# Kernel tuning notes

Measured on AMD Instinct MI355X. Metric: run time of the kernel, lower is better.

Reference implementation:

```python
import jax, jax.numpy as jnp
import numpy as np

B, S, HID, H = 4, 2048, 768, 12
D = HID // H  # 64
SCALE = 1.0 / (D ** 0.5)


def setup_inputs() -> dict:
    key = jax.random.key(0)
    ks = jax.random.split(key, 12)
    std = 0.02
    inp = {
        'Q': jax.random.normal(ks[0], (B, S, HID), jnp.float32),
        'K': jax.random.normal(ks[1], (B, S, HID), jnp.float32),
        'V': jax.random.normal(ks[2], (B, S, HID), jnp.float32),
        'attn_mask': jax.random.randint(ks[3], (B, S, S), 0, 2) == 1,
        'Wq': jax.random.normal(ks[4], (HID, HID), jnp.float32) * std,
        'bq': jnp.zeros((HID,), jnp.float32),
        'Wk': jax.random.normal(ks[5], (HID, HID), jnp.float32) * std,
        'bk': jnp.zeros((HID,), jnp.float32),
        'Wv': jax.random.normal(ks[6], (HID, HID), jnp.float32) * std,
        'bv': jnp.zeros((HID,), jnp.float32),
        'Wo': jax.random.normal(ks[7], (HID, HID), jnp.float32) * std,
        'bo': jnp.zeros((HID,), jnp.float32),
    }
    return inp


def reference(Q, K, V, attn_mask, Wq, bq, Wk, bk, Wv, bv, Wo, bo):
    b, s, _ = Q.shape
    # projections -> [b, h, s, d]
    def split_heads(x):
        return x.reshape(b, s, H, D).transpose(0, 2, 1, 3)
    q = split_heads(Q @ Wq + bq)
    k = split_heads(K @ Wk + bk)
    v = split_heads(V @ Wv + bv)
    # eager attention: materialize full [b,h,s,s] scores
    scores = jnp.einsum('bhqd,bhkd->bhqk', q, k) * SCALE
    scores = jnp.where(attn_mask[:, None, :, :], jnp.float32(-1e9), scores)
    attn_prob = jax.nn.softmax(scores, axis=-1)
    # dropout is identity in eval mode
    context = jnp.einsum('bhqk,bhkd->bhqd', attn_prob, v)
    context = context.transpose(0, 2, 1, 3).reshape(b, s, H * D)
    output = context @ Wo + bo
    return (output, attn_prob)
```

## Files before the change

kernel.cpp:

```cpp
#include <hip/hip_runtime.h>
#include <hip/hip_bf16.h>
#include <stdint.h>

#define BB 4
#define SS 2048
#define HIDD 768
#define HH 12
#define DD 64
#define SCALE_F 0.125f
#define NQKV ((size_t)BB * SS * HIDD)
#define NW ((size_t)HIDD * HIDD)
#define NMW ((size_t)BB * SS * (SS / 64))

using bf16 = __hip_bfloat16;
typedef __attribute__((ext_vector_type(8))) short short8v;
typedef __attribute__((ext_vector_type(4))) float f32x4;
typedef __attribute__((ext_vector_type(4))) float fvec4;
typedef __attribute__((ext_vector_type(4))) unsigned int uvec4;

__device__ __forceinline__ float ldf(const float* p, size_t i) { return p[i]; }
__device__ __forceinline__ float ldf(const bf16* p, size_t i) { return __bfloat162float(p[i]); }

__device__ __forceinline__ uint32_t bfb(float f) {
    bf16 h = __float2bfloat16(f);
    uint16_t u;
    __builtin_memcpy(&u, &h, 2);
    return (uint32_t)u;
}
__device__ __forceinline__ float b2f(uint32_t u) {
    uint32_t w = u << 16;
    float f;
    __builtin_memcpy(&f, &w, 4);
    return f;
}
__device__ __forceinline__ uint4 load8p(const float* p) {
    float4 a = *(const float4*)p;
    float4 b = *(const float4*)(p + 4);
    uint4 r;
    r.x = bfb(a.x) | (bfb(a.y) << 16);
    r.y = bfb(a.z) | (bfb(a.w) << 16);
    r.z = bfb(b.x) | (bfb(b.y) << 16);
    r.w = bfb(b.z) | (bfb(b.w) << 16);
    return r;
}

__device__ __forceinline__ short8v ldfrag(const char* base, int row, int bofs) {
    return *(const short8v*)(base + row * 128 + (bofs ^ ((row & 7) << 4)));
}

typedef __attribute__((address_space(1))) void as1_void;
typedef __attribute__((address_space(3))) void as3_void;
__device__ __forceinline__ void gload16(const void* g, void* l) {
    __builtin_amdgcn_global_load_lds((as1_void*)g, (as3_void*)l, 16, 0, 0);
}

__global__ void detect_kernel(const uint32_t* __restrict__ qraw,
                              const uint32_t* __restrict__ mraw,
                              int* __restrict__ flags) {
    __shared__ int ci, cn;
    int tid = threadIdx.x;
    if (tid == 0) { ci = 0; cn = 0; }
    __syncthreads();
    int li = 0;
    for (int l = 0; l < 8; l++) {
        uint32_t w = qraw[tid + l * 256];
        #pragma unroll
        for (int h = 0; h < 2; h++) {
            uint32_t bits = (h ? (w >> 16) : (w & 0xffffu)) << 16;
            float f = __uint_as_float(bits);
            float a = fabsf(f);
            if (a != 0.0f && (a > 1e3f || a < 1e-4f)) li++;
        }
    }
    int ln = 0;
    for (int l = 0; l < 4; l++) {
        if (mraw[tid + l * 256] > 1u) ln++;
    }
    atomicAdd(&ci, li);
    atomicAdd(&cn, ln);
    __syncthreads();
    if (tid == 0) {
        flags[0] = (ci > 1024) ? 0 : 1;
        flags[1] = (cn > 64) ? 1 : 0;
    }
}

__global__ __launch_bounds__(256) void bitpack_mask(const int* __restrict__ flags,
                                                    const void* __restrict__ maskp,
                                                    uint64_t* __restrict__ mbits) {
    int gw = (int)((blockIdx.x * 256 + threadIdx.x) >> 6);
    int lane = threadIdx.x & 63;
    int byteM = flags[1];
    const int* mi = (const int*)maskp;
    const uint8_t* mb = (const uint8_t*)maskp;
    for (int it = 0; it < 64; it++) {
        size_t wi = (size_t)gw * 64 + it;
        size_t e = wi * 64 + lane;
        int m = byteM ? (int)mb[e] : mi[e];
        unsigned long long b = __ballot(m != 0);
        if (lane == 0) mbits[wi] = (uint64_t)b;
    }
}

__global__ __launch_bounds__(256) void convert_in(const int* __restrict__ flags,
                                                  const void* __restrict__ Q,
                                                  const void* __restrict__ K,
                                                  const void* __restrict__ V,
                                                  bf16* __restrict__ xb) {
    int isbf = flags[0];
    int z = blockIdx.y;
    const void* src = (z == 0) ? Q : (z == 1) ? K : V;
    size_t base = ((size_t)blockIdx.x * 256 + threadIdx.x) * 8;
    bf16* dst = xb + (size_t)z * NQKV + base;
    if (isbf) {
        *(uint4*)dst = *(const uint4*)((const bf16*)src + base);
    } else {
        *(uint4*)dst = load8p((const float*)src + base);
    }
}

__global__ void convert_bias(const int* __restrict__ flags,
                             const void* __restrict__ b0, const void* __restrict__ b1,
                             const void* __restrict__ b2, const void* __restrict__ b3,
                             float* __restrict__ bf) {
    int isbf = flags[0];
    for (int i = threadIdx.x; i < 4 * HIDD; i += 256) {
        int z = i / HIDD, j = i - z * HIDD;
        const void* b = (z == 0) ? b0 : (z == 1) ? b1 : (z == 2) ? b2 : b3;
        bf[i] = isbf ? b2f((uint32_t) * ((const uint16_t*)b + j)) : ((const float*)b)[j];
    }
}

__global__ __launch_bounds__(256) void transpose_w2(const int* __restrict__ flags,
                                                    const void* __restrict__ W0,
                                                    const void* __restrict__ W1,
                                                    const void* __restrict__ W2,
                                                    const void* __restrict__ W3,
                                                    bf16* __restrict__ WT) {
    int isbf = flags[0];
    __shared__ uint16_t tb[64][65];
    int tid = threadIdx.x;
    int z = blockIdx.z;
    const void* W = (z == 0) ? W0 : (z == 1) ? W1 : (z == 2) ? W2 : W3;
    int k0 = blockIdx.y * 64, n0 = blockIdx.x * 64;
    #pragma unroll
    for (int l = 0; l < 16; l++) {
        int idx = tid + l * 256;
        int r = idx >> 6, c = idx & 63;
        size_t off = (size_t)(k0 + r) * HIDD + n0 + c;
        tb[c][r] = isbf ? *((const uint16_t*)W + off) : (uint16_t)bfb(((const float*)W)[off]);
    }
    __syncthreads();
    bf16* dst = WT + (size_t)z * NW;
    #pragma unroll
    for (int l = 0; l < 16; l++) {
        int idx = tid + l * 256;
        int r = idx >> 6, c = idx & 63;
        *(uint16_t*)&dst[(size_t)(n0 + r) * HIDD + k0 + c] = tb[r][c];
    }
}

template <int HSPLIT>
__global__ __launch_bounds__(256) void gemm3(const int* __restrict__ flags,
                                             const bf16* __restrict__ X,
                                             const bf16* __restrict__ WT,
                                             const float* __restrict__ biasf,
                                             bf16* __restrict__ Yh,
                                             float* __restrict__ Yf,
                                             bf16* __restrict__ Yb) {
    __shared__ char xs[128 * 128];
    __shared__ char ws[64 * 128];
    int tid = threadIdx.x;
    int lane = tid & 63, w = tid >> 6;
    int g = lane >> 4, t = lane & 15;
    int row0 = blockIdx.y * 128, n0 = blockIdx.x * 64;
    const f32x4 fz = {0.f, 0.f, 0.f, 0.f};
    f32x4 acc[2][4];
    #pragma unroll
    for (int rb = 0; rb < 2; rb++)
        #pragma unroll
        for (int c = 0; c < 4; c++) acc[rb][c] = fz;
    int r8 = tid >> 3, c8 = tid & 7;
    const char* Xb0 = (const char*)(X + (size_t)row0 * HIDD);
    const char* Wb0 = (const char*)(WT + (size_t)n0 * HIDD);
    for (int kt = 0; kt < HIDD; kt += 64) {
        #pragma unroll
        for (int i = 0; i < 4; i++) {
            int r = r8 + i * 32;
            gload16(Xb0 + (size_t)r * (HIDD * 2) + kt * 2 + ((c8 * 16) ^ ((r & 7) << 4)),
                    xs + w * 1024 + i * 4096);
        }
        #pragma unroll
        for (int i = 0; i < 2; i++) {
            int r = r8 + i * 32;
            gload16(Wb0 + (size_t)r * (HIDD * 2) + kt * 2 + ((c8 * 16) ^ ((r & 7) << 4)),
                    ws + w * 1024 + i * 4096);
        }
        __syncthreads();
        #pragma unroll
        for (int ks = 0; ks < 2; ks++) {
            short8v a0 = ldfrag(xs, w * 32 + t, g * 16 + ks * 64);
            short8v a1 = ldfrag(xs, w * 32 + 16 + t, g * 16 + ks * 64);
            #pragma unroll
            for (int c = 0; c < 4; c++) {
                short8v b = ldfrag(ws, c * 16 + t, g * 16 + ks * 64);
                acc[0][c] = __builtin_amdgcn_mfma_f32_16x16x32_bf16(a0, b, acc[0][c], 0, 0, 0);
                acc[1][c] = __builtin_amdgcn_mfma_f32_16x16x32_bf16(a1, b, acc[1][c], 0, 0, 0);
            }
        }
        __syncthreads();
    }
    int isbf = flags[0];
    #pragma unroll
    for (int c = 0; c < 4; c++) {
        int col = n0 + c * 16 + t;
        float bv = biasf[col];
        #pragma unroll
        for (int rb = 0; rb < 2; rb++) {
            #pragma unroll
            for (int r = 0; r < 4; r++) {
                int row = row0 + w * 32 + rb * 16 + g * 4 + r;
                float v = acc[rb][c][r] + bv;
                if (HSPLIT) {
                    int b_ = row >> 11, s = row & 2047, h2 = col >> 6, d = col & 63;
                    Yh[(((size_t)b_ * HH + h2) * SS + s) * DD + d] = __float2bfloat16(v);
                } else {
                    if (isbf) Yb[(size_t)row * HIDD + col] = __float2bfloat16(v);
                    else      Yf[(size_t)row * HIDD + col] = v;
                }
            }
        }
    }
}

__global__ __launch_bounds__(256) void transpose_v(const bf16* __restrict__ vh,
                                                   bf16* __restrict__ vt) {
    __shared__ uint16_t tb[64][65];
    int tid = threadIdx.x;
    int s0 = blockIdx.x * 64, bh = blockIdx.y;
    const bf16* src = vh + ((size_t)bh * SS + s0) * DD;
    #pragma unroll
    for (int i = 0; i < 2; i++) {
        int u = tid + (i << 8);
        int r = u >> 3, sg = u & 7;
        uint4 v = *(const uint4*)(src + (size_t)r * DD + sg * 8);
        uint32_t wv[4] = {v.x, v.y, v.z, v.w};
        #pragma unroll
        for (int j = 0; j < 4; j++) {
            tb[r][sg * 8 + 2 * j]     = (uint16_t)(wv[j] & 0xffffu);
            tb[r][sg * 8 + 2 * j + 1] = (uint16_t)(wv[j] >> 16);
        }
    }
    __syncthreads();
    bf16* dst = vt + (size_t)bh * DD * SS + s0;
    #pragma unroll
    for (int i = 0; i < 2; i++) {
        int u = tid + (i << 8);
        int d = u >> 3, sg = u & 7;
        uint32_t w0 = (uint32_t)tb[sg * 8 + 0][d] | ((uint32_t)tb[sg * 8 + 1][d] << 16);
        uint32_t w1 = (uint32_t)tb[sg * 8 + 2][d] | ((uint32_t)tb[sg * 8 + 3][d] << 16);
        uint32_t w2 = (uint32_t)tb[sg * 8 + 4][d] | ((uint32_t)tb[sg * 8 + 5][d] << 16);
        uint32_t w3 = (uint32_t)tb[sg * 8 + 6][d] | ((uint32_t)tb[sg * 8 + 7][d] << 16);
        uint4 o; o.x = w0; o.y = w1; o.z = w2; o.w = w3;
        *(uint4*)(dst + (size_t)d * SS + sg * 8) = o;
    }
}

__global__ __launch_bounds__(256) void fused_attn3(const int* __restrict__ flags,
                                                   const bf16* __restrict__ qh,
                                                   const bf16* __restrict__ kh,
                                                   const bf16* __restrict__ vt,
                                                   const uint64_t* __restrict__ mbits,
                                                   float* __restrict__ Pf,
                                                   bf16* __restrict__ Ph,
                                                   bf16* __restrict__ ctx) {
    const int isf32 = (flags[0] == 0);
    __shared__ char pl[16 * 4096];
    __shared__ float red[4][16];
    __shared__ float invl[16];
    int tid = threadIdx.x;
    int lane = tid & 63, w = tid >> 6;
    int g = lane >> 4, t = lane & 15;
    int q0 = blockIdx.x * 16, bh = blockIdx.y;
    int b_ = bh / HH, h = bh - b_ * HH;
    const f32x4 fz = {0.f, 0.f, 0.f, 0.f};
    int bitIdx = w * 16 + t;

    const bf16* qbase = qh + ((size_t)bh * SS + q0 + t) * DD;
    short8v aq0 = *(const short8v*)(qbase + g * 8);
    short8v aq1 = *(const short8v*)(qbase + 32 + g * 8);

    const bf16* kcol = kh + ((size_t)bh * SS + bitIdx) * DD + g * 8;
    const bf16* vrow = vt + ((size_t)bh * DD + bitIdx) * SS + g * 8;
    const uint64_t* mrowp[4];
    #pragma unroll
    for (int r = 0; r < 4; r++)
        mrowp[r] = mbits + ((size_t)b_ * SS + q0 + g * 4 + r) * (SS / 64);

    short8v cK0 = *(const short8v*)(kcol);
    short8v cK1 = *(const short8v*)(kcol + 32);
    short8v cV0 = *(const short8v*)(vrow);
    short8v cV1 = *(const short8v*)(vrow + 32);
    uint64_t cM[4];
    #pragma unroll
    for (int r = 0; r < 4; r++) cM[r] = mrowp[r][0];

    float sum4[4] = {0.f, 0.f, 0.f, 0.f};
    f32x4 o = fz;

    for (int kt = 0; kt < SS; kt += 64) {
        int ktn = (kt + 64) & (SS - 1);
        const bf16* kn = kcol + (size_t)ktn * DD;
        const bf16* vn = vrow + ktn;
        short8v nK0 = *(const short8v*)(kn);
        short8v nK1 = *(const short8v*)(kn + 32);
        short8v nV0 = *(const short8v*)(vn);
        short8v nV1 = *(const short8v*)(vn + 32);
        int wn = ((kt >> 6) + 1) & 31;
        uint64_t nM[4];
        #pragma unroll
        for (int r = 0; r < 4; r++) nM[r] = mrowp[r][wn];

        f32x4 s = fz;
        s = __builtin_amdgcn_mfma_f32_16x16x32_bf16(aq0, cK0, s, 0, 0, 0);
        s = __builtin_amdgcn_mfma_f32_16x16x32_bf16(aq1, cK1, s, 0, 0, 0);

        #pragma unroll
        for (int r = 0; r < 4; r++) {
            int msk = (int)((cM[r] >> bitIdx) & 1ull);
            float sv = msk ? -1e30f : s[r] * SCALE_F;
            float p = __expf(fminf(sv, 30.0f));
            sum4[r] += p;
            int row = g * 4 + r;
            int colb = (kt + bitIdx) * 2;
            *(uint16_t*)(pl + row * 4096 + (colb ^ ((row & 7) << 4))) = (uint16_t)bfb(p);
        }

        asm volatile("s_waitcnt lgkmcnt(0)" ::: "memory");
        __builtin_amdgcn_s_barrier();
        asm volatile("" ::: "memory");
        __builtin_amdgcn_sched_barrier(0);

        short8v ap0 = *(const short8v*)(pl + t * 4096 + (((kt + g * 8) * 2) ^ ((t & 7) << 4)));
        short8v ap1 = *(const short8v*)(pl + t * 4096 + (((kt + 32 + g * 8) * 2) ^ ((t & 7) << 4)));
        o = __builtin_amdgcn_mfma_f32_16x16x32_bf16(ap0, cV0, o, 0, 0, 0);
        o = __builtin_amdgcn_mfma_f32_16x16x32_bf16(ap1, cV1, o, 0, 0, 0);

        cK0 = nK0; cK1 = nK1; cV0 = nV0; cV1 = nV1;
        #pragma unroll
        for (int r = 0; r < 4; r++) cM[r] = nM[r];
    }

    #pragma unroll
    for (int r = 0; r < 4; r++) {
        float v = sum4[r];
        #pragma unroll
        for (int d = 1; d < 16; d <<= 1) v += __shfl_xor(v, d);
        if (t == 0) red[w][g * 4 + r] = v;
    }
    __syncthreads();
    if (tid < 16) {
        float tot = red[0][tid] + red[1][tid] + red[2][tid] + red[3][tid];
        invl[tid] = (tot > 0.f) ? 1.0f / tot : 0.0f;
    }
    __syncthreads();

    #pragma unroll
    for (int r = 0; r < 4; r++) {
        int q = q0 + g * 4 + r;
        ctx[((size_t)b_ * SS + q) * HIDD + h * DD + bitIdx] =
            __float2bfloat16(o[r] * invl[g * 4 + r]);
    }

    int prow = tid >> 4, cg = tid & 15;
    float pinv = invl[prow];
    size_t rowb = ((size_t)bh * SS + q0 + prow) * SS;
    if (isf32) {
        #pragma unroll
        for (int c0 = 0; c0 < SS; c0 += 128) {
            int col = c0 + cg * 8;
            uint4 pv = *(const uint4*)(pl + prow * 4096 + ((col * 2) ^ ((prow & 7) << 4)));
            fvec4 lo = {b2f(pv.x & 0xffffu) * pinv, b2f(pv.x >> 16) * pinv,
                        b2f(pv.y & 0xffffu) * pinv, b2f(pv.y >> 16) * pinv};
            fvec4 hi = {b2f(pv.z & 0xffffu) * pinv, b2f(pv.z >> 16) * pinv,
                        b2f(pv.w & 0xffffu) * pinv, b2f(pv.w >> 16) * pinv};
            __builtin_nontemporal_store(lo, (fvec4*)(Pf + rowb + col));
            __builtin_nontemporal_store(hi, (fvec4*)(Pf + rowb + col + 4));
        }
    } else {
        #pragma unroll
        for (int c0 = 0; c0 < SS; c0 += 128) {
            int col = c0 + cg * 8;
            uint4 pv = *(const uint4*)(pl + prow * 4096 + ((col * 2) ^ ((prow & 7) << 4)));
            uvec4 ov;
            ov.x = bfb(b2f(pv.x & 0xffffu) * pinv) | (bfb(b2f(pv.x >> 16) * pinv) << 16);
            ov.y = bfb(b2f(pv.y & 0xffffu) * pinv) | (bfb(b2f(pv.y >> 16) * pinv) << 16);
            ov.z = bfb(b2f(pv.z & 0xffffu) * pinv) | (bfb(b2f(pv.z >> 16) * pinv) << 16);
            ov.w = bfb(b2f(pv.w & 0xffffu) * pinv) | (bfb(b2f(pv.w >> 16) * pinv) << 16);
            __builtin_nontemporal_store(ov, (uvec4*)(Ph + rowb + col));
        }
    }
}

extern "C" void kernel_launch(void* const* d_in, const int* in_sizes, int n_in,
                              void* d_out, int out_size, void* d_ws, size_t ws_size,
                              hipStream_t stream) {
    bf16* qh = (bf16*)d_ws;
    bf16* kh = qh + NQKV;
    bf16* vh = kh + NQKV;
    bf16* vt = vh + NQKV;
    bf16* WT = vt + NQKV;
    uint64_t* mbits = (uint64_t*)(WT + 4 * NW);
    int* flags = (int*)(mbits + NMW);
    float* bfp = (float*)(flags + 4);
    bf16* ctx = vh;

    bf16* xb = (bf16*)((char*)d_out + NQKV * 4);

    detect_kernel<<<1, 256, 0, stream>>>((const uint32_t*)d_in[0], (const uint32_t*)d_in[3], flags);
    bitpack_mask<<<1024, 256, 0, stream>>>(flags, d_in[3], mbits);
    convert_in<<<dim3(3072, 3), 256, 0, stream>>>(flags, d_in[0], d_in[1], d_in[2], xb);
    convert_bias<<<1, 256, 0, stream>>>(flags, d_in[5], d_in[7], d_in[9], d_in[11], bfp);
    transpose_w2<<<dim3(12, 12, 4), 256, 0, stream>>>(flags, d_in[4], d_in[6], d_in[8],
                                                      d_in[10], WT);

    dim3 blk(256);
    dim3 gG(HIDD / 64, (BB * SS) / 128);
    dim3 gT(SS / 64, BB * HH);
    dim3 gF(SS / 16, BB * HH);

    gemm3<1><<<gG, blk, 0, stream>>>(flags, xb + 0 * NQKV, WT + 0 * NW, bfp + 0 * HIDD,
                                     qh, nullptr, nullptr);
    gemm3<1><<<gG, blk, 0, stream>>>(flags, xb + 1 * NQKV, WT + 1 * NW, bfp + 1 * HIDD,
                                     kh, nullptr, nullptr);
    gemm3<1><<<gG, blk, 0, stream>>>(flags, xb + 2 * NQKV, WT + 2 * NW, bfp + 2 * HIDD,
                                     vh, nullptr, nullptr);

    transpose_v<<<gT, blk, 0, stream>>>(vh, vt);

    fused_attn3<<<gF, blk, 0, stream>>>(flags, qh, kh, vt, mbits,
                                        (float*)d_out + NQKV, (bf16*)d_out + NQKV, ctx);

    gemm3<0><<<gG, blk, 0, stream>>>(flags, ctx, WT + 3 * NW, bfp + 3 * HIDD,
                                     nullptr, (float*)d_out, (bf16*)d_out);
}
```

Before: 1.466 ms.

## Restructure attention to keep P in registers and batch QKV GEMMs

The fused attention kernel now computes S transposed (K as the A operand), so each wave handles 128 keys per iteration and feeds its probabilities straight from registers into the PV MFMA across all 64 head dims. This removes the per-tile LDS round trip and barrier that the old version needed before PV. Partial context sums from the four waves are then reduced through LDS at the end. Separately, the three Q/K/V projection GEMMs are merged into one launch using blockIdx.z, which cuts launch overhead and lets the three projections share the GPU at once.

```diff
diff --git a/kernel.cpp b/kernel.cpp
--- a/kernel.cpp
+++ b/kernel.cpp
@@ -18,9 +18,6 @@
 typedef __attribute__((ext_vector_type(4))) float fvec4;
 typedef __attribute__((ext_vector_type(4))) unsigned int uvec4;
 
-__device__ __forceinline__ float ldf(const float* p, size_t i) { return p[i]; }
-__device__ __forceinline__ float ldf(const bf16* p, size_t i) { return __bfloat162float(p[i]); }
-
 __device__ __forceinline__ uint32_t bfb(float f) {
     bf16 h = __float2bfloat16(f);
     uint16_t u;
@@ -42,6 +39,11 @@
     r.z = bfb(b.x) | (bfb(b.y) << 16);
     r.w = bfb(b.z) | (bfb(b.w) << 16);
     return r;
+}
+__device__ __forceinline__ short8v mk8(uint2 a, uint2 b) {
+    union { short8v v; uint4 u; } x;
+    x.u.x = a.x; x.u.y = a.y; x.u.z = b.x; x.u.w = b.y;
+    return x.v;
 }
 
 __device__ __forceinline__ short8v ldfrag(const char* base, int row, int bofs) {
@@ -168,6 +170,11 @@
                                              bf16* __restrict__ Yh,
                                              float* __restrict__ Yf,
                                              bf16* __restrict__ Yb) {
+    int z = blockIdx.z;
+    X += (size_t)z * NQKV;
+    WT += (size_t)z * NW;
+    biasf += (size_t)z * HIDD;
+    if (HSPLIT) Yh += (size_t)z * NQKV;
     __shared__ char xs[128 * 128];
     __shared__ char ws[64 * 128];
     int tid = threadIdx.x;
@@ -266,7 +273,7 @@
     }
 }
 
-__global__ __launch_bounds__(256) void fused_attn3(const int* __restrict__ flags,
+__global__ __launch_bounds__(256) void fused_attn4(const int* __restrict__ flags,
                                                    const bf16* __restrict__ qh,
                                                    const bf16* __restrict__ kh,
                                                    const bf16* __restrict__ vt,
@@ -284,93 +291,99 @@
     int q0 = blockIdx.x * 16, bh = blockIdx.y;
     int b_ = bh / HH, h = bh - b_ * HH;
     const f32x4 fz = {0.f, 0.f, 0.f, 0.f};
-    int bitIdx = w * 16 + t;
+    int sh = w * 16 + g * 4;
 
     const bf16* qbase = qh + ((size_t)bh * SS + q0 + t) * DD;
-    short8v aq0 = *(const short8v*)(qbase + g * 8);
-    short8v aq1 = *(const short8v*)(qbase + 32 + g * 8);
-
-    const bf16* kcol = kh + ((size_t)bh * SS + bitIdx) * DD + g * 8;
-    const bf16* vrow = vt + ((size_t)bh * DD + bitIdx) * SS + g * 8;
-    const uint64_t* mrowp[4];
-    #pragma unroll
-    for (int r = 0; r < 4; r++)
-        mrowp[r] = mbits + ((size_t)b_ * SS + q0 + g * 4 + r) * (SS / 64);
-
-    short8v cK0 = *(const short8v*)(kcol);
-    short8v cK1 = *(const short8v*)(kcol + 32);
-    short8v cV0 = *(const short8v*)(vrow);
-    short8v cV1 = *(const short8v*)(vrow + 32);
-    uint64_t cM[4];
-    #pragma unroll
-    for (int r = 0; r < 4; r++) cM[r] = mrowp[r][0];
-
-    float sum4[4] = {0.f, 0.f, 0.f, 0.f};
-    f32x4 o = fz;
-
-    for (int kt = 0; kt < SS; kt += 64) {
-        int ktn = (kt + 64) & (SS - 1);
-        const bf16* kn = kcol + (size_t)ktn * DD;
-        const bf16* vn = vrow + ktn;
-        short8v nK0 = *(const short8v*)(kn);
-        short8v nK1 = *(const short8v*)(kn + 32);
-        short8v nV0 = *(const short8v*)(vn);
-        short8v nV1 = *(const short8v*)(vn + 32);
-        int wn = ((kt >> 6) + 1) & 31;
-        uint64_t nM[4];
-        #pragma unroll
-        for (int r = 0; r < 4; r++) nM[r] = mrowp[r][wn];
-
-        f32x4 s = fz;
-        s = __builtin_amdgcn_mfma_f32_16x16x32_bf16(aq0, cK0, s, 0, 0, 0);
-        s = __builtin_amdgcn_mfma_f32_16x16x32_bf16(aq1, cK1, s, 0, 0, 0);
-
+    short8v bq0 = *(const short8v*)(qbase + g * 8);
+    short8v bq1 = *(const short8v*)(qbase + 32 + g * 8);
+
+    const bf16* kb = kh + ((size_t)bh * SS + w * 16 + t) * DD + g * 8;
+    const bf16* vbr = vt + ((size_t)bh * DD + t) * SS + sh;
+    const uint64_t* mrow = mbits + ((size_t)b_ * SS + q0 + t) * (SS / 64);
+
+    short8v cK00 = *(const short8v*)(kb);
+    short8v cK01 = *(const short8v*)(kb + 32);
+    short8v cK10 = *(const short8v*)(kb + 64 * DD);
+    short8v cK11 = *(const short8v*)(kb + 64 * DD + 32);
+    uint4 cMM = *(const uint4*)(mrow);
+    uint2 cV[4][2];
+    #pragma unroll
+    for (int db = 0; db < 4; db++) {
+        cV[db][0] = *(const uint2*)(vbr + (size_t)db * 16 * SS);
+        cV[db][1] = *(const uint2*)(vbr + (size_t)db * 16 * SS + 64);
+    }
+
+    float sum = 0.f;
+    f32x4 o[4] = {fz, fz, fz, fz};
+
+    for (int it = 0; it < 16; ++it) {
+        int ni = (it + 1) & 15;
+        const bf16* knb = kb + (size_t)ni * 128 * DD;
+        short8v nK00 = *(const short8v*)(knb);
+        short8v nK01 = *(const short8v*)(knb + 32);
+        short8v nK10 = *(const short8v*)(knb + 64 * DD);
+        short8v nK11 = *(const short8v*)(knb + 64 * DD + 32);
+        uint4 nMM = *(const uint4*)(mrow + ni * 2);
+        uint2 nV[4][2];
+        #pragma unroll
+        for (int db = 0; db < 4; db++) {
+            nV[db][0] = *(const uint2*)(vbr + (size_t)db * 16 * SS + ni * 128);
+            nV[db][1] = *(const uint2*)(vbr + (size_t)db * 16 * SS + ni * 128 + 64);
+        }
+
+        f32x4 s0 = fz, s1 = fz;
+        s0 = __builtin_amdgcn_mfma_f32_16x16x32_bf16(cK00, bq0, s0, 0, 0, 0);
+        s0 = __builtin_amdgcn_mfma_f32_16x16x32_bf16(cK01, bq1, s0, 0, 0, 0);
+        s1 = __builtin_amdgcn_mfma_f32_16x16x32_bf16(cK10, bq0, s1, 0, 0, 0);
+        s1 = __builtin_amdgcn_mfma_f32_16x16x32_bf16(cK11, bq1, s1, 0, 0, 0);
+
+        uint64_t M0 = ((uint64_t)cMM.y << 32) | cMM.x;
+        uint64_t M1 = ((uint64_t)cMM.w << 32) | cMM.z;
+        uint32_t mb0 = (uint32_t)(M0 >> sh) & 0xFu;
+        uint32_t mb1 = (uint32_t)(M1 >> sh) & 0xFu;
+        float p0[4], p1[4];
         #pragma unroll
         for (int r = 0; r < 4; r++) {
-            int msk = (int)((cM[r] >> bitIdx) & 1ull);
-            float sv = msk ? -1e30f : s[r] * SCALE_F;
-            float p = __expf(fminf(sv, 30.0f));
-            sum4[r] += p;
-            int row = g * 4 + r;
-            int colb = (kt + bitIdx) * 2;
-            *(uint16_t*)(pl + row * 4096 + (colb ^ ((row & 7) << 4))) = (uint16_t)bfb(p);
-        }
-
-        asm volatile("s_waitcnt lgkmcnt(0)" ::: "memory");
-        __builtin_amdgcn_s_barrier();
-        asm volatile("" ::: "memory");
-        __builtin_amdgcn_sched_barrier(0);
-
-        short8v ap0 = *(const short8v*)(pl + t * 4096 + (((kt + g * 8) * 2) ^ ((t & 7) << 4)));
-        short8v ap1 = *(const short8v*)(pl + t * 4096 + (((kt + 32 + g * 8) * 2) ^ ((t & 7) << 4)));
-        o = __builtin_amdgcn_mfma_f32_16x16x32_bf16(ap0, cV0, o, 0, 0, 0);
-        o = __builtin_amdgcn_mfma_f32_16x16x32_bf16(ap1, cV1, o, 0, 0, 0);
-
-        cK0 = nK0; cK1 = nK1; cV0 = nV0; cV1 = nV1;
-        #pragma unroll
-        for (int r = 0; r < 4; r++) cM[r] = nM[r];
-    }
-
-    #pragma unroll
-    for (int r = 0; r < 4; r++) {
-        float v = sum4[r];
-        #pragma unroll
-        for (int d = 1; d < 16; d <<= 1) v += __shfl_xor(v, d);
-        if (t == 0) red[w][g * 4 + r] = v;
-    }
+            float sv0 = ((mb0 >> r) & 1u) ? -1e30f : s0[r] * SCALE_F;
+            p0[r] = __expf(fminf(sv0, 30.0f));
+            float sv1 = ((mb1 >> r) & 1u) ? -1e30f : s1[r] * SCALE_F;
+            p1[r] = __expf(fminf(sv1, 30.0f));
+            sum += p0[r] + p1[r];
+        }
+
+        uint2 pw0, pw1;
+        pw0.x = bfb(p0[0]) | (bfb(p0[1]) << 16);
+        pw0.y = bfb(p0[2]) | (bfb(p0[3]) << 16);
+        pw1.x = bfb(p1[0]) | (bfb(p1[1]) << 16);
+        pw1.y = bfb(p1[2]) | (bfb(p1[3]) << 16);
+        int ts0 = it * 128;
+        int k0b = (ts0 + sh) * 2, k1b = (ts0 + 64 + sh) * 2;
+        *(uint2*)(pl + t * 4096 + (k0b ^ ((t & 7) << 4))) = pw0;
+        *(uint2*)(pl + t * 4096 + (k1b ^ ((t & 7) << 4))) = pw1;
+
+        short8v pa = mk8(pw0, pw1);
+        #pragma unroll
+        for (int db = 0; db < 4; db++) {
+            o[db] = __builtin_amdgcn_mfma_f32_16x16x32_bf16(pa, mk8(cV[db][0], cV[db][1]),
+                                                            o[db], 0, 0, 0);
+        }
+
+        cK00 = nK00; cK01 = nK01; cK10 = nK10; cK11 = nK11;
+        cMM = nMM;
+        #pragma unroll
+        for (int db = 0; db < 4; db++) { cV[db][0] = nV[db][0]; cV[db][1] = nV[db][1]; }
+    }
+
+    float sg = sum;
+    sg += __shfl_xor(sg, 16);
+    sg += __shfl_xor(sg, 32);
+    if (lane < 16) red[w][lane] = sg;
     __syncthreads();
     if (tid < 16) {
         float tot = red[0][tid] + red[1][tid] + red[2][tid] + red[3][tid];
         invl[tid] = (tot > 0.f) ? 1.0f / tot : 0.0f;
     }
     __syncthreads();
-
-    #pragma unroll
-    for (int r = 0; r < 4; r++) {
-        int q = q0 + g * 4 + r;
-        ctx[((size_t)b_ * SS + q) * HIDD + h * DD + bitIdx] =
-            __float2bfloat16(o[r] * invl[g * 4 + r]);
-    }
 
     int prow = tid >> 4, cg = tid & 15;
     float pinv = invl[prow];
@@ -400,6 +413,27 @@
             __builtin_nontemporal_store(ov, (uvec4*)(Ph + rowb + col));
         }
     }
+    __syncthreads();
+
+    float* ored = (float*)pl;
+    #pragma unroll
+    for (int db = 0; db < 4; db++)
+        #pragma unroll
+        for (int r = 0; r < 4; r++)
+            ored[(w * 16 + g * 4 + r) * 65 + db * 16 + t] = o[db][r];
+    __syncthreads();
+    int qq = tid >> 4, d4 = (tid & 15) * 4;
+    float iv = invl[qq];
+    float cj[4];
+    #pragma unroll
+    for (int j = 0; j < 4; j++) {
+        cj[j] = (ored[(0 * 16 + qq) * 65 + d4 + j] + ored[(1 * 16 + qq) * 65 + d4 + j] +
+                 ored[(2 * 16 + qq) * 65 + d4 + j] + ored[(3 * 16 + qq) * 65 + d4 + j]) * iv;
+    }
+    uint2 cw;
+    cw.x = bfb(cj[0]) | (bfb(cj[1]) << 16);
+    cw.y = bfb(cj[2]) | (bfb(cj[3]) << 16);
+    *(uint2*)&ctx[((size_t)b_ * SS + q0 + qq) * HIDD + h * DD + d4] = cw;
 }
 
 extern "C" void kernel_launch(void* const* d_in, const int* in_sizes, int n_in,
@@ -425,22 +459,18 @@
                                                       d_in[10], WT);
 
     dim3 blk(256);
-    dim3 gG(HIDD / 64, (BB * SS) / 128);
+    dim3 gG(HIDD / 64, (BB * SS) / 128, 3);
+    dim3 gO(HIDD / 64, (BB * SS) / 128, 1);
     dim3 gT(SS / 64, BB * HH);
     dim3 gF(SS / 16, BB * HH);
 
-    gemm3<1><<<gG, blk, 0, stream>>>(flags, xb + 0 * NQKV, WT + 0 * NW, bfp + 0 * HIDD,
-                                     qh, nullptr, nullptr);
-    gemm3<1><<<gG, blk, 0, stream>>>(flags, xb + 1 * NQKV, WT + 1 * NW, bfp + 1 * HIDD,
-                                     kh, nullptr, nullptr);
-    gemm3<1><<<gG, blk, 0, stream>>>(flags, xb + 2 * NQKV, WT + 2 * NW, bfp + 2 * HIDD,
-                                     vh, nullptr, nullptr);
+    gemm3<1><<<gG, blk, 0, stream>>>(flags, xb, WT, bfp, qh, nullptr, nullptr);
 
     transpose_v<<<gT, blk, 0, stream>>>(vh, vt);
 
-    fused_attn3<<<gF, blk, 0, stream>>>(flags, qh, kh, vt, mbits,
+    fused_attn4<<<gF, blk, 0, stream>>>(flags, qh, kh, vt, mbits,
                                         (float*)d_out + NQKV, (bf16*)d_out + NQKV, ctx);
 
-    gemm3<0><<<gG, blk, 0, stream>>>(flags, ctx, WT + 3 * NW, bfp + 3 * HIDD,
+    gemm3<0><<<gO, blk, 0, stream>>>(flags, ctx, WT + 3 * NW, bfp + 3 * HIDD,
                                      nullptr, (float*)d_out, (bf16*)d_out);
 }
```

After: 1.529 ms. +4.4%, slower.
